# Performance work log

Measured on AMD Instinct MI355X. Metric: run time of the kernel, lower is better.

## Reference

```python
import jax, jax.numpy as jnp
import numpy as np

BN_EPS = 1e-5

def setup_inputs() -> dict:
    key = jax.random.key(0)
    k1, k2, k3 = jax.random.split(key, 3)
    N, F, H, E = 50000, 256, 256, 1600000
    x = jax.random.normal(k1, (N, F), dtype=jnp.float32)
    edge_index = jax.random.randint(k2, (2, E), 0, N, dtype=jnp.int64)
    # Linear(F, H) params, PyTorch default init scale
    lim = 1.0 / np.sqrt(F)
    W = jax.random.uniform(k3, (H, F), dtype=jnp.float32, minval=-lim, maxval=lim)
    b = jnp.zeros((H,), dtype=jnp.float32)
    bn_w = jnp.ones((H,), dtype=jnp.float32)
    bn_b = jnp.zeros((H,), dtype=jnp.float32)
    return {"x": x, "edge_index": edge_index, "W": W, "b": b, "bn_w": bn_w, "bn_b": bn_b}

def reference(x, edge_index, W, b, bn_w, bn_b):
    N = x.shape[0]
    src, dst = edge_index[0], edge_index[1]
    # GIN aggregation: sum of neighbor features (messages flow src -> dst)
    agg = jax.ops.segment_sum(x[src], dst, num_segments=N)
    h = x + agg  # (1 + eps) * x + agg, eps = 0
    # MLP: Linear then BatchNorm1d (training mode: batch stats, biased var)
    h = jnp.einsum('nf,hf->nh', h, W) + b
    mean = jnp.mean(h, axis=0)
    var = jnp.mean(jnp.square(h - mean), axis=0)
    out = (h - mean) * jax.lax.rsqrt(var + BN_EPS) * bn_w + bn_b
    return out
```

## Files before the change

kernel.cpp:

```cpp
#include <hip/hip_runtime.h>

#define NN 50000
#define FDIM 256
#define HDIM 256
#define BN_EPS 1e-5f
#define RB 32
#define KC 16
#define NP 264
#define SCAN_CHUNK 1024
#define NBLK_SCAN ((NN + SCAN_CHUNK - 1) / SCAN_CHUNK)

#define BKT 32
#define NBKT 1563
#define ECAP 1280
#define PFB 256
#define SBUF_CAP 6400
#define PSC_NPT 7
#define PAIR_SRC(p) (((p) >> 5) & 0xFFFFu)
#define PAIR_LDST(p) ((p) & 31u)

typedef __attribute__((ext_vector_type(8))) short short8v;
typedef __attribute__((ext_vector_type(8))) unsigned short ushort8v;
typedef __attribute__((ext_vector_type(4))) float f32x4;

__device__ __forceinline__ float b2f(unsigned short u) {
    return __uint_as_float(((unsigned)u) << 16);
}
__device__ __forceinline__ unsigned short f2b(float f) {
    unsigned u = __float_as_uint(f);
    return (unsigned short)((u + 0x7FFFu + ((u >> 16) & 1u)) >> 16);
}

__global__ void k_cvt2(const float4* __restrict__ x, const float4* __restrict__ W,
                       ushort4* __restrict__ xb, ushort4* __restrict__ Wb,
                       int nx4, int nw4) {
    int i = blockIdx.x * blockDim.x + threadIdx.x;
    if (i < nx4) {
        float4 v = x[i];
        xb[i] = make_ushort4(f2b(v.x), f2b(v.y), f2b(v.z), f2b(v.w));
    } else {
        int j = i - nx4;
        if (j < nw4) {
            float4 v = W[j];
            Wb[j] = make_ushort4(f2b(v.x), f2b(v.y), f2b(v.z), f2b(v.w));
        }
    }
}

__launch_bounds__(256)
__global__ void k_phist(const int* __restrict__ dst, int* __restrict__ bcnt, int E) {
    __shared__ int lhist[NBKT];
    int t = threadIdx.x;
    int chunk = (E + 255) / 256;
    int c0 = blockIdx.x * chunk;
    int c1 = min(E, c0 + chunk);
    for (int i = t; i < NBKT; i += 256) lhist[i] = 0;
    __syncthreads();
    for (int e = c0 + t; e < c1; e += 256) atomicAdd(&lhist[dst[e] >> 5], 1);
    __syncthreads();
    for (int i = t; i < NBKT; i += 256) {
        int h = lhist[i];
        if (h) atomicAdd(&bcnt[i], h);
    }
}

__global__ void k_pscan(const int* __restrict__ bcnt, int* __restrict__ bbase,
                        int* __restrict__ bcursor) {
    __shared__ int ts[256];
    int t = threadIdx.x;
    int i0 = t * PSC_NPT;
    int s = 0;
    for (int i = 0; i < PSC_NPT; i++) {
        int idx = i0 + i;
        if (idx < NBKT) s += bcnt[idx];
    }
    ts[t] = s;
    __syncthreads();
    for (int off = 1; off < 256; off <<= 1) {
        int val = (t >= off) ? ts[t - off] : 0;
        __syncthreads();
        ts[t] += val;
        __syncthreads();
    }
    int run = ts[t] - s;
    for (int i = 0; i < PSC_NPT; i++) {
        int idx = i0 + i;
        if (idx < NBKT) {
            bbase[idx] = run;
            bcursor[idx] = run;
            run += bcnt[idx];
        }
    }
}

__launch_bounds__(256)
__global__ void k_pfill_sort(const int* __restrict__ src, const int* __restrict__ dst,
                             int* __restrict__ bcursor, unsigned int* __restrict__ pairs,
                             int E) {
    __shared__ int lhist[NBKT];
    __shared__ int lofs[NBKT];
    __shared__ int ts[256];
    __shared__ unsigned int sbuf[SBUF_CAP];
    int t = threadIdx.x;
    int chunk = (E + PFB - 1) / PFB;
    int c0 = blockIdx.x * chunk;
    int c1 = min(E, c0 + chunk);
    int n = c1 - c0;

    for (int i = t; i < NBKT; i += 256) lhist[i] = 0;
    __syncthreads();
    for (int e = c0 + t; e < c1; e += 256) atomicAdd(&lhist[dst[e] >> 5], 1);
    __syncthreads();
    {
        int i0 = t * PSC_NPT;
        int s = 0;
        int loc[PSC_NPT];
        for (int i = 0; i < PSC_NPT; i++) {
            int idx = i0 + i;
            loc[i] = (idx < NBKT) ? lhist[idx] : 0;
            s += loc[i];
        }
        ts[t] = s;
        __syncthreads();
        for (int off = 1; off < 256; off <<= 1) {
            int val = (t >= off) ? ts[t - off] : 0;
            __syncthreads();
            ts[t] += val;
            __syncthreads();
        }
        int run = ts[t] - s;
        for (int i = 0; i < PSC_NPT; i++) {
            int idx = i0 + i;
            if (idx < NBKT) {
                lofs[idx] = run;
                run += loc[i];
            }
        }
    }
    __syncthreads();
    if (t < 256) {}
    for (int i = t; i < NBKT; i += 256) lhist[i] = lofs[i];
    __syncthreads();
    for (int e = c0 + t; e < c1; e += 256) {
        int d = dst[e];
        unsigned bkt = (unsigned)d >> 5;
        int rank = atomicAdd(&lhist[bkt], 1);
        sbuf[rank] = (bkt << 21) | ((unsigned)src[e] << 5) | ((unsigned)d & 31u);
    }
    __syncthreads();
    for (int i = t; i < NBKT; i += 256) {
        int cnt = lhist[i] - lofs[i];
        int gb = cnt ? atomicAdd(&bcursor[i], cnt) : 0;
        lhist[i] = gb - lofs[i];
    }
    __syncthreads();
    for (int j = t; j < n; j += 256) {
        unsigned int p = sbuf[j];
        pairs[j + lhist[p >> 21]] = p;
    }
}

__launch_bounds__(256)
__global__ void k_pfill(const int* __restrict__ src, const int* __restrict__ dst,
                        int* __restrict__ bcursor, unsigned int* __restrict__ pairs, int E) {
    __shared__ int lhist[NBKT];
    __shared__ int lbase[NBKT];
    int t = threadIdx.x;
    int chunk = (E + PFB - 1) / PFB;
    int c0 = blockIdx.x * chunk;
    int c1 = min(E, c0 + chunk);
    for (int i = t; i < NBKT; i += 256) lhist[i] = 0;
    __syncthreads();
    for (int e = c0 + t; e < c1; e += 256) atomicAdd(&lhist[dst[e] >> 5], 1);
    __syncthreads();
    for (int i = t; i < NBKT; i += 256) {
        int h = lhist[i];
        lbase[i] = h ? atomicAdd(&bcursor[i], h) : 0;
        lhist[i] = 0;
    }
    __syncthreads();
    for (int e = c0 + t; e < c1; e += 256) {
        int d = dst[e];
        unsigned bkt = (unsigned)d >> 5;
        int rank = atomicAdd(&lhist[bkt], 1);
        pairs[lbase[bkt] + rank] = (bkt << 21) | ((unsigned)src[e] << 5) | ((unsigned)d & 31u);
    }
}

__launch_bounds__(256, 6)
__global__ void k_agg_gemm(const ushort4* __restrict__ xb4, const unsigned int* __restrict__ pairs,
                           const int* __restrict__ bbase, const int* __restrict__ bcnt,
                           const unsigned short* __restrict__ Wb, const float* __restrict__ bias,
                           unsigned short* __restrict__ hb, float* __restrict__ stat) {
    __shared__ unsigned int lp[ECAP];
    __shared__ int lhist[BKT];
    __shared__ int lofs[BKT + 1];
    __shared__ unsigned short As[BKT * NP];
    __shared__ float ssum[HDIM];
    __shared__ float ssq[HDIM];
    const int t = threadIdx.x;
    const int lane = t & 63;
    const int wid = t >> 6;
    const int q = lane >> 4;
    const int l16 = lane & 15;
    const int v0 = blockIdx.x * BKT;
    const int ebeg = bbase[blockIdx.x];
    const int ecnt = bcnt[blockIdx.x];
    const int vrows = min(BKT, NN - v0);

    ssum[t] = 0.f;
    ssq[t] = 0.f;

    if (ecnt <= ECAP) {
        if (t < BKT) lhist[t] = 0;
        __syncthreads();
        for (int e = t; e < ecnt; e += 256)
            atomicAdd(&lhist[PAIR_LDST(pairs[ebeg + e])], 1);
        __syncthreads();
        if (t == 0) {
            int run = 0;
            for (int r = 0; r < BKT; r++) { lofs[r] = run; run += lhist[r]; }
            lofs[BKT] = run;
        }
        __syncthreads();
        if (t < BKT) lhist[t] = lofs[t];
        __syncthreads();
        for (int e = t; e < ecnt; e += 256) {
            unsigned int p = pairs[ebeg + e];
            int pos = atomicAdd(&lhist[PAIR_LDST(p)], 1);
            lp[pos] = p;
        }
        __syncthreads();
#pragma unroll
        for (int i = 0; i < 8; i++) {
            int r = wid * 8 + i;
            int v = v0 + r;
            if (v < NN) {
                ushort4 u0 = xb4[(size_t)v * 64 + lane];
                float a0 = b2f(u0.x), a1 = b2f(u0.y), a2 = b2f(u0.z), a3 = b2f(u0.w);
                int e0 = __builtin_amdgcn_readfirstlane(lofs[r]);
                int e1 = __builtin_amdgcn_readfirstlane(lofs[r + 1]);
                int e = e0;
                for (; e + 16 <= e1; e += 16) {
                    ushort4 u[16];
#pragma unroll
                    for (int j = 0; j < 16; j++)
                        u[j] = xb4[(size_t)PAIR_SRC(lp[e + j]) * 64 + lane];
#pragma unroll
                    for (int j = 0; j < 16; j++) {
                        a0 += b2f(u[j].x); a1 += b2f(u[j].y);
                        a2 += b2f(u[j].z); a3 += b2f(u[j].w);
                    }
                }
                for (; e + 4 <= e1; e += 4) {
                    ushort4 ua = xb4[(size_t)PAIR_SRC(lp[e]) * 64 + lane];
                    ushort4 ub = xb4[(size_t)PAIR_SRC(lp[e + 1]) * 64 + lane];
                    ushort4 uc = xb4[(size_t)PAIR_SRC(lp[e + 2]) * 64 + lane];
                    ushort4 ud = xb4[(size_t)PAIR_SRC(lp[e + 3]) * 64 + lane];
                    a0 += (b2f(ua.x) + b2f(ub.x)) + (b2f(uc.x) + b2f(ud.x));
                    a1 += (b2f(ua.y) + b2f(ub.y)) + (b2f(uc.y) + b2f(ud.y));
                    a2 += (b2f(ua.z) + b2f(ub.z)) + (b2f(uc.z) + b2f(ud.z));
                    a3 += (b2f(ua.w) + b2f(ub.w)) + (b2f(uc.w) + b2f(ud.w));
                }
                for (; e < e1; e++) {
                    ushort4 ua = xb4[(size_t)PAIR_SRC(lp[e]) * 64 + lane];
                    a0 += b2f(ua.x); a1 += b2f(ua.y); a2 += b2f(ua.z); a3 += b2f(ua.w);
                }
                *(ushort4*)(As + r * NP + lane * 4) =
                    make_ushort4(f2b(a0), f2b(a1), f2b(a2), f2b(a3));
            } else {
                *(ushort4*)(As + r * NP + lane * 4) = make_ushort4(0, 0, 0, 0);
            }
        }
    } else {
#pragma unroll
        for (int i = 0; i < 8; i++) {
            int r = wid * 8 + i;
            int v = v0 + r;
            float a0 = 0.f, a1 = 0.f, a2 = 0.f, a3 = 0.f;
            if (v < NN) {
                ushort4 u0 = xb4[(size_t)v * 64 + lane];
                a0 = b2f(u0.x); a1 = b2f(u0.y); a2 = b2f(u0.z); a3 = b2f(u0.w);
                for (int e = 0; e < ecnt; e++) {
                    unsigned int p = pairs[ebeg + e];
                    if ((int)PAIR_LDST(p) == r) {
                        ushort4 cu = xb4[(size_t)PAIR_SRC(p) * 64 + lane];
                        a0 += b2f(cu.x); a1 += b2f(cu.y); a2 += b2f(cu.z); a3 += b2f(cu.w);
                    }
                }
            }
            *(ushort4*)(As + r * NP + lane * 4) =
                make_ushort4(f2b(a0), f2b(a1), f2b(a2), f2b(a3));
        }
    }
    __syncthreads();

    f32x4 acc[2][4];
#pragma unroll
    for (int mt = 0; mt < 2; mt++)
#pragma unroll
        for (int nt = 0; nt < 4; nt++) acc[mt][nt] = (f32x4)0.f;

    const int w = wid;
#pragma unroll
    for (int ks = 0; ks < 8; ks++) {
        const int kk = ks * 32;
        short8v af[2], bf_[4];
#pragma unroll
        for (int mt = 0; mt < 2; mt++)
            af[mt] = *(const short8v*)(As + (mt * 16 + l16) * NP + kk + q * 8);
#pragma unroll
        for (int nt = 0; nt < 4; nt++)
            bf_[nt] = *(const short8v*)(Wb + (size_t)(w * 64 + nt * 16 + l16) * FDIM + kk + q * 8);
#pragma unroll
        for (int mt = 0; mt < 2; mt++)
#pragma unroll
            for (int nt = 0; nt < 4; nt++)
                acc[mt][nt] = __builtin_amdgcn_mfma_f32_16x16x32_bf16(af[mt], bf_[nt], acc[mt][nt], 0, 0, 0);
    }

#pragma unroll
    for (int nt = 0; nt < 4; nt++) {
        const int col = w * 64 + nt * 16 + l16;
        const float bcol = bias[col];
        float s = 0.f, qq = 0.f;
#pragma unroll
        for (int mt = 0; mt < 2; mt++) {
            const int rbase = mt * 16 + q * 4;
#pragma unroll
            for (int r = 0; r < 4; r++) {
                int row = rbase + r;
                if (row < vrows) {
                    float v = acc[mt][nt][r] + bcol;
                    hb[(size_t)(v0 + row) * FDIM + col] = f2b(v);
                    s += v;
                    qq += v * v;
                }
            }
        }
        atomicAdd(&ssum[col], s);
        atomicAdd(&ssq[col], qq);
    }
    __syncthreads();
    atomicAdd(&stat[t], ssum[t]);
    atomicAdd(&stat[256 + t], ssq[t]);
}

__global__ void k_final(const float* __restrict__ stat, const float* __restrict__ bn_w,
                        const float* __restrict__ bn_b, float* __restrict__ ss) {
    int j = threadIdx.x;
    const float inv_n = 1.0f / (float)NN;
    float mean = stat[j] * inv_n;
    float var = stat[256 + j] * inv_n - mean * mean;
    float sc = bn_w[j] * rsqrtf(var + BN_EPS);
    ss[j] = sc;
    ss[256 + j] = bn_b[j] - mean * sc;
}

__global__ void k_norm8(const ushort8v* __restrict__ hb8, const float* __restrict__ ss,
                        float4* __restrict__ out, int n8) {
    int i = blockIdx.x * blockDim.x + threadIdx.x;
    if (i >= n8) return;
    ushort8v u = hb8[i];
    int c8 = (i & 31) << 3;
    float4 sc0 = *(const float4*)(ss + c8);
    float4 sc1 = *(const float4*)(ss + c8 + 4);
    float4 sh0 = *(const float4*)(ss + 256 + c8);
    float4 sh1 = *(const float4*)(ss + 256 + c8 + 4);
    float4 v0, v1;
    v0.x = fmaf(b2f(u[0]), sc0.x, sh0.x);
    v0.y = fmaf(b2f(u[1]), sc0.y, sh0.y);
    v0.z = fmaf(b2f(u[2]), sc0.z, sh0.z);
    v0.w = fmaf(b2f(u[3]), sc0.w, sh0.w);
    v1.x = fmaf(b2f(u[4]), sc1.x, sh1.x);
    v1.y = fmaf(b2f(u[5]), sc1.y, sh1.y);
    v1.z = fmaf(b2f(u[6]), sc1.z, sh1.z);
    v1.w = fmaf(b2f(u[7]), sc1.w, sh1.w);
    out[i * 2 + 0] = v0;
    out[i * 2 + 1] = v1;
}

__global__ void k_hist(const int* __restrict__ dst, int* __restrict__ cnt, int E) {
    int e = blockIdx.x * blockDim.x + threadIdx.x;
    if (e < E) atomicAdd(&cnt[dst[e]], 1);
}
__global__ void k_scan1(const int* __restrict__ cnt, int* __restrict__ offs,
                        int* __restrict__ bsum) {
    __shared__ int ts[256];
    int t = threadIdx.x;
    int base = blockIdx.x * SCAN_CHUNK + t * 4;
    int v0 = (base + 0 < NN) ? cnt[base + 0] : 0;
    int v1 = (base + 1 < NN) ? cnt[base + 1] : 0;
    int v2 = (base + 2 < NN) ? cnt[base + 2] : 0;
    int v3 = (base + 3 < NN) ? cnt[base + 3] : 0;
    int tsum = v0 + v1 + v2 + v3;
    ts[t] = tsum;
    __syncthreads();
    for (int off = 1; off < 256; off <<= 1) {
        int val = (t >= off) ? ts[t - off] : 0;
        __syncthreads();
        ts[t] += val;
        __syncthreads();
    }
    int excl = ts[t] - tsum;
    if (t == 255) bsum[blockIdx.x] = ts[255];
    if (base + 0 < NN) offs[base + 0] = excl;
    if (base + 1 < NN) offs[base + 1] = excl + v0;
    if (base + 2 < NN) offs[base + 2] = excl + v0 + v1;
    if (base + 3 < NN) offs[base + 3] = excl + v0 + v1 + v2;
}
__global__ void k_scan2(int* __restrict__ bsum, int nb) {
    if (threadIdx.x == 0 && blockIdx.x == 0) {
        int run = 0;
        for (int i = 0; i < nb; i++) { int v = bsum[i]; bsum[i] = run; run += v; }
    }
}
__global__ void k_scan3(int* __restrict__ offs, const int* __restrict__ bsum,
                        int* __restrict__ cursor) {
    int i = blockIdx.x * blockDim.x + threadIdx.x;
    if (i >= NN) return;
    int o = offs[i] + bsum[i >> 10];
    offs[i] = o;
    cursor[i] = o;
}
__global__ void k_bucket(const int* __restrict__ src, const int* __restrict__ dst,
                         int* __restrict__ cursor, int* __restrict__ csr, int E) {
    int e = blockIdx.x * blockDim.x + threadIdx.x;
    if (e >= E) return;
    int pos = atomicAdd(&cursor[dst[e]], 1);
    csr[pos] = src[e];
}
__global__ void k_copy(const float4* __restrict__ x, float4* __restrict__ out, int n4) {
    int i = blockIdx.x * blockDim.x + threadIdx.x;
    if (i < n4) out[i] = x[i];
}
__global__ void k_scatter(const float* __restrict__ x, const int* __restrict__ src,
                          const int* __restrict__ dst, float* __restrict__ out, int E) {
    int t = blockIdx.x * blockDim.x + threadIdx.x;
    int e = t >> 6;
    if (e >= E) return;
    int c = (t & 63) << 2;
    long s = src[e], d = dst[e];
    const float4 v = *(const float4*)(x + s * FDIM + c);
    float* o = out + d * FDIM + c;
    atomicAdd(o + 0, v.x);
    atomicAdd(o + 1, v.y);
    atomicAdd(o + 2, v.z);
    atomicAdd(o + 3, v.w);
}
__launch_bounds__(256)
__global__ void k_gather(const float4* __restrict__ x, const int* __restrict__ offs,
                         const int* __restrict__ cnt, const int* __restrict__ csr,
                         float4* __restrict__ out) {
    int v = blockIdx.x * 4 + (threadIdx.x >> 6);
    if (v >= NN) return;
    int lane = threadIdx.x & 63;
    int beg = __builtin_amdgcn_readfirstlane(offs[v]);
    int d   = __builtin_amdgcn_readfirstlane(cnt[v]);
    float4 acc = x[(size_t)v * 64 + lane];
    int i = 0;
    for (; i + 4 <= d; i += 4) {
        int s0 = csr[beg + i], s1 = csr[beg + i + 1];
        int s2 = csr[beg + i + 2], s3 = csr[beg + i + 3];
        float4 a = x[(size_t)s0 * 64 + lane];
        float4 b = x[(size_t)s1 * 64 + lane];
        float4 c = x[(size_t)s2 * 64 + lane];
        float4 e = x[(size_t)s3 * 64 + lane];
        acc.x += (a.x + b.x) + (c.x + e.x);
        acc.y += (a.y + b.y) + (c.y + e.y);
        acc.z += (a.z + b.z) + (c.z + e.z);
        acc.w += (a.w + b.w) + (c.w + e.w);
    }
    for (; i < d; i++) {
        int s = csr[beg + i];
        float4 a = x[(size_t)s * 64 + lane];
        acc.x += a.x; acc.y += a.y; acc.z += a.z; acc.w += a.w;
    }
    out[(size_t)v * 64 + lane] = acc;
}
__launch_bounds__(256)
__global__ void k_gemm_stats(float* __restrict__ h,
                             const float* __restrict__ W,
                             const float* __restrict__ bias,
                             float* __restrict__ stat) {
    __shared__ float hs[RB * FDIM];
    __shared__ float wt[KC * HDIM];
    const int j = threadIdx.x;
    const int c = j & 63;
    const int g = j >> 6;
    const long row0 = (long)blockIdx.x * RB;
    const int vrows = min(RB, NN - (int)row0);
    const int vf4 = vrows * (FDIM / 4);

    float4* hsv = (float4*)hs;
    const float4* hv = (const float4*)(h + row0 * FDIM);
#pragma unroll
    for (int i = 0; i < (RB * FDIM / 4) / 256; i++) {
        int f4 = j + i * 256;
        hsv[f4] = (f4 < vf4) ? hv[f4] : make_float4(0.f, 0.f, 0.f, 0.f);
    }
    __syncthreads();

    float acc[8][4];
#pragma unroll
    for (int r = 0; r < 8; r++)
#pragma unroll
        for (int qi = 0; qi < 4; qi++) acc[r][qi] = 0.f;

    for (int kb = 0; kb < FDIM; kb += KC) {
        __syncthreads();
#pragma unroll
        for (int i = 0; i < KC / 4; i++) {
            float4 w4 = *(const float4*)(W + (size_t)j * FDIM + kb + i * 4);
            wt[(i * 4 + 0) * HDIM + j] = w4.x;
            wt[(i * 4 + 1) * HDIM + j] = w4.y;
            wt[(i * 4 + 2) * HDIM + j] = w4.z;
            wt[(i * 4 + 3) * HDIM + j] = w4.w;
        }
        __syncthreads();
#pragma unroll
        for (int k = 0; k < KC; k++) {
            float4 wv = *(const float4*)(wt + k * HDIM + c * 4);
#pragma unroll
            for (int r = 0; r < 8; r++) {
                float hval = hs[(g * 8 + r) * FDIM + kb + k];
                acc[r][0] = fmaf(hval, wv.x, acc[r][0]);
                acc[r][1] = fmaf(hval, wv.y, acc[r][1]);
                acc[r][2] = fmaf(hval, wv.z, acc[r][2]);
                acc[r][3] = fmaf(hval, wv.w, acc[r][3]);
            }
        }
    }
    __syncthreads();
    wt[j] = 0.f;
    wt[256 + j] = 0.f;
    __syncthreads();

    float4 bv = *(const float4*)(bias + c * 4);
    float s0 = 0, s1 = 0, s2 = 0, s3 = 0, q0 = 0, q1 = 0, q2 = 0, q3 = 0;
#pragma unroll
    for (int r = 0; r < 8; r++) {
        int row = g * 8 + r;
        if (row < vrows) {
            float4 v;
            v.x = acc[r][0] + bv.x;
            v.y = acc[r][1] + bv.y;
            v.z = acc[r][2] + bv.z;
            v.w = acc[r][3] + bv.w;
            *(float4*)(h + (row0 + row) * FDIM + c * 4) = v;
            s0 += v.x; s1 += v.y; s2 += v.z; s3 += v.w;
            q0 += v.x * v.x; q1 += v.y * v.y; q2 += v.z * v.z; q3 += v.w * v.w;
        }
    }
    atomicAdd(&wt[c * 4 + 0], s0);
    atomicAdd(&wt[c * 4 + 1], s1);
    atomicAdd(&wt[c * 4 + 2], s2);
    atomicAdd(&wt[c * 4 + 3], s3);
    atomicAdd(&wt[256 + c * 4 + 0], q0);
    atomicAdd(&wt[256 + c * 4 + 1], q1);
    atomicAdd(&wt[256 + c * 4 + 2], q2);
    atomicAdd(&wt[256 + c * 4 + 3], q3);
    __syncthreads();
    atomicAdd(&stat[j], wt[j]);
    atomicAdd(&stat[256 + j], wt[256 + j]);
}
__global__ void k_norm(float* __restrict__ out, const float* __restrict__ ss, int n4) {
    int i = blockIdx.x * blockDim.x + threadIdx.x;
    if (i >= n4) return;
    float4 v = ((float4*)out)[i];
    int c4 = (i & 63) << 2;
    float4 sc = *(const float4*)(ss + c4);
    float4 sh = *(const float4*)(ss + 256 + c4);
    v.x = fmaf(v.x, sc.x, sh.x);
    v.y = fmaf(v.y, sc.y, sh.y);
    v.z = fmaf(v.z, sc.z, sh.z);
    v.w = fmaf(v.w, sc.w, sh.w);
    ((float4*)out)[i] = v;
}

extern "C" void kernel_launch(void* const* d_in, const int* in_sizes, int n_in,
                              void* d_out, int out_size, void* d_ws, size_t ws_size,
                              hipStream_t stream) {
    const float* x   = (const float*)d_in[0];
    const int*   ei  = (const int*)d_in[1];
    const float* W   = (const float*)d_in[2];
    const float* b   = (const float*)d_in[3];
    const float* bnw = (const float*)d_in[4];
    const float* bnb = (const float*)d_in[5];
    float* out = (float*)d_out;
    char* ws = (char*)d_ws;
    const int E = in_sizes[1] / 2;
    const int n4 = NN * FDIM / 4;
    const int n8 = NN * FDIM / 8;
    const int* src = ei;
    const int* dst = ei + E;

    size_t off = 0;
    float* stat = (float*)(ws + off);          off += 4096;
    int* bcnt   = (int*)(ws + off);            off += 8192;
    int* bbase  = (int*)(ws + off);            off += 8192;
    int* bcur   = (int*)(ws + off);            off += 8192;
    unsigned int* pairs = (unsigned int*)(ws + off); off += (size_t)E * 4;
    off = (off + 255) & ~(size_t)255;
    unsigned short* Wb = (unsigned short*)(ws + off); off += 131072;
    unsigned short* xb = (unsigned short*)(ws + off); off += (size_t)NN * FDIM * 2;
    unsigned short* hb = (unsigned short*)(ws + off); off += (size_t)NN * FDIM * 2;
    const size_t need_fast = off;

    size_t foff = 0;
    float* fstat  = (float*)(ws + foff); foff += 4096;
    int*   cnt    = (int*)(ws + foff);   foff += 204800;
    int*   offs   = (int*)(ws + foff);   foff += 204800;
    int*   cursor = (int*)(ws + foff);   foff += 204800;
    int*   bsum   = (int*)(ws + foff);   foff += 4096;
    int*   csr    = (int*)(ws + foff);   foff += (size_t)E * 4;
    const size_t need_mid = foff;

    const bool src_fits = (NN <= 65536);

    if (ws_size >= need_fast && src_fits) {
        hipMemsetAsync(stat, 0, 2 * 256 * sizeof(float), stream);
        hipMemsetAsync(bcnt, 0, NBKT * sizeof(int), stream);
        const int nw4 = HDIM * FDIM / 4;
        k_cvt2<<<(n4 + nw4 + 255) / 256, 256, 0, stream>>>((const float4*)x, (const float4*)W,
                                                           (ushort4*)xb, (ushort4*)Wb, n4, nw4);
        k_phist<<<256, 256, 0, stream>>>(dst, bcnt, E);
        k_pscan<<<1, 256, 0, stream>>>(bcnt, bbase, bcur);
        const int chunk = (E + PFB - 1) / PFB;
        if (chunk <= SBUF_CAP)
            k_pfill_sort<<<PFB, 256, 0, stream>>>(src, dst, bcur, pairs, E);
        else
            k_pfill<<<PFB, 256, 0, stream>>>(src, dst, bcur, pairs, E);
        k_agg_gemm<<<NBKT, 256, 0, stream>>>((const ushort4*)xb, pairs, bbase, bcnt,
                                             Wb, b, hb, stat);
        k_final<<<1, 256, 0, stream>>>(stat, bnw, bnb, stat + 512);
        k_norm8<<<(n8 + 255) / 256, 256, 0, stream>>>((const ushort8v*)hb, stat + 512,
                                                      (float4*)out, n8);
    } else if (ws_size >= need_mid) {
        hipMemsetAsync(fstat, 0, 2 * 256 * sizeof(float), stream);
        hipMemsetAsync(cnt, 0, NN * sizeof(int), stream);
        k_hist<<<(E + 255) / 256, 256, 0, stream>>>(dst, cnt, E);
        k_scan1<<<NBLK_SCAN, 256, 0, stream>>>(cnt, offs, bsum);
        k_scan2<<<1, 64, 0, stream>>>(bsum, NBLK_SCAN);
        k_scan3<<<(NN + 255) / 256, 256, 0, stream>>>(offs, bsum, cursor);
        k_bucket<<<(E + 255) / 256, 256, 0, stream>>>(src, dst, cursor, csr, E);
        k_gather<<<(NN + 3) / 4, 256, 0, stream>>>((const float4*)x, offs, cnt, csr,
                                                   (float4*)out);
        k_gemm_stats<<<(NN + RB - 1) / RB, 256, 0, stream>>>(out, W, b, fstat);
        k_final<<<1, 256, 0, stream>>>(fstat, bnw, bnb, fstat + 512);
        k_norm<<<(n4 + 255) / 256, 256, 0, stream>>>(out, fstat + 512, n4);
    } else {
        hipMemsetAsync(fstat, 0, 2 * 256 * sizeof(float), stream);
        k_copy<<<(n4 + 255) / 256, 256, 0, stream>>>((const float4*)x, (float4*)out, n4);
        long threads = (long)E * 64;
        k_scatter<<<(int)((threads + 255) / 256), 256, 0, stream>>>(x, src, dst, out, E);
        k_gemm_stats<<<(NN + RB - 1) / RB, 256, 0, stream>>>(out, W, b, fstat);
        k_final<<<1, 256, 0, stream>>>(fstat, bnw, bnb, fstat + 512);
        k_norm<<<(n4 + 255) / 256, 256, 0, stream>>>(out, fstat + 512, n4);
    }
}
```

Before: 326.6 us.

## Split fused aggregate-GEMM into CSR column-sliced gather plus separate MFMA GEMM

Adds a new default path that builds a per-node CSR through hist/scan/bucket, then gathers neighbor rows in 32-column slices so each block touches only a slice of xb, which is meant to improve cache reuse. A separate bf16 MFMA GEMM kernel computes the batch-norm statistics. The memsets are folded into the conversion kernel and scan2 now stages through shared memory. The cost is an extra round trip of the aggregated bf16 hb buffer through memory and atomic-based bucketing in place of the bucketed pair sort.

```diff
diff --git a/kernel.cpp b/kernel.cpp
--- a/kernel.cpp
+++ b/kernel.cpp
@@ -19,9 +19,13 @@
 #define PAIR_SRC(p) (((p) >> 5) & 0xFFFFu)
 #define PAIR_LDST(p) ((p) & 31u)
 
+#define NSLC 8
+#define AGG_BLOCKS 1536
+
 typedef __attribute__((ext_vector_type(8))) short short8v;
 typedef __attribute__((ext_vector_type(8))) unsigned short ushort8v;
 typedef __attribute__((ext_vector_type(4))) float f32x4;
+typedef __attribute__((ext_vector_type(4))) unsigned short us4;
 
 __device__ __forceinline__ float b2f(unsigned short u) {
     return __uint_as_float(((unsigned)u) << 16);
@@ -45,6 +49,239 @@
             Wb[j] = make_ushort4(f2b(v.x), f2b(v.y), f2b(v.z), f2b(v.w));
         }
     }
+}
+
+__global__ void k_cvt2z(const float4* __restrict__ x, const float4* __restrict__ W,
+                        ushort4* __restrict__ xb, ushort4* __restrict__ Wb,
+                        int nx4, int nw4, float* __restrict__ stat, int* __restrict__ cnt) {
+    int i = blockIdx.x * blockDim.x + threadIdx.x;
+    if (i < NN) cnt[i] = 0;
+    if (i < 512) stat[i] = 0.f;
+    if (i < nx4) {
+        float4 v = x[i];
+        xb[i] = make_ushort4(f2b(v.x), f2b(v.y), f2b(v.z), f2b(v.w));
+    } else {
+        int j = i - nx4;
+        if (j < nw4) {
+            float4 v = W[j];
+            Wb[j] = make_ushort4(f2b(v.x), f2b(v.y), f2b(v.z), f2b(v.w));
+        }
+    }
+}
+
+__global__ void k_hist(const int* __restrict__ dst, int* __restrict__ cnt, int E) {
+    int e = blockIdx.x * blockDim.x + threadIdx.x;
+    if (e < E) atomicAdd(&cnt[dst[e]], 1);
+}
+__global__ void k_scan1(const int* __restrict__ cnt, int* __restrict__ offs,
+                        int* __restrict__ bsum) {
+    __shared__ int ts[256];
+    int t = threadIdx.x;
+    int base = blockIdx.x * SCAN_CHUNK + t * 4;
+    int v0 = (base + 0 < NN) ? cnt[base + 0] : 0;
+    int v1 = (base + 1 < NN) ? cnt[base + 1] : 0;
+    int v2 = (base + 2 < NN) ? cnt[base + 2] : 0;
+    int v3 = (base + 3 < NN) ? cnt[base + 3] : 0;
+    int tsum = v0 + v1 + v2 + v3;
+    ts[t] = tsum;
+    __syncthreads();
+    for (int off = 1; off < 256; off <<= 1) {
+        int val = (t >= off) ? ts[t - off] : 0;
+        __syncthreads();
+        ts[t] += val;
+        __syncthreads();
+    }
+    int excl = ts[t] - tsum;
+    if (t == 255) bsum[blockIdx.x] = ts[255];
+    if (base + 0 < NN) offs[base + 0] = excl;
+    if (base + 1 < NN) offs[base + 1] = excl + v0;
+    if (base + 2 < NN) offs[base + 2] = excl + v0 + v1;
+    if (base + 3 < NN) offs[base + 3] = excl + v0 + v1 + v2;
+}
+__global__ void k_scan2(int* __restrict__ bsum, int nb) {
+    __shared__ int s[64];
+    int t = threadIdx.x;
+    s[t] = (t < nb) ? bsum[t] : 0;
+    __syncthreads();
+    if (t == 0) {
+        int run = 0;
+        for (int i = 0; i < nb; i++) { int v = s[i]; s[i] = run; run += v; }
+    }
+    __syncthreads();
+    if (t < nb) bsum[t] = s[t];
+}
+__global__ void k_scan3(int* __restrict__ offs, const int* __restrict__ bsum,
+                        int* __restrict__ cursor, int E) {
+    int i = blockIdx.x * blockDim.x + threadIdx.x;
+    if (i == 0) offs[NN] = E;
+    if (i >= NN) return;
+    int o = offs[i] + bsum[i >> 10];
+    offs[i] = o;
+    cursor[i] = o;
+}
+__global__ void k_bucket(const int* __restrict__ src, const int* __restrict__ dst,
+                         int* __restrict__ cursor, int* __restrict__ csr, int E) {
+    int e = blockIdx.x * blockDim.x + threadIdx.x;
+    if (e >= E) return;
+    int pos = atomicAdd(&cursor[dst[e]], 1);
+    csr[pos] = src[e];
+}
+
+__launch_bounds__(256, 6)
+__global__ void k_agg_slice(const unsigned short* __restrict__ xb,
+                            const int* __restrict__ srcs,
+                            const int* __restrict__ offs,
+                            unsigned short* __restrict__ hb) {
+    const int t = threadIdx.x;
+    const int lane = t & 63;
+    const int wid = t >> 6;
+    const int sg = lane >> 3;
+    const int qd = lane & 7;
+    const int slice = blockIdx.x & 7;
+    const int cb = slice * 32 + qd * 4;
+    const int nper = gridDim.x >> 3;
+    for (int tile = blockIdx.x >> 3; tile < NBKT; tile += nper) {
+        const int v = tile * BKT + wid * 8 + sg;
+        if (v >= NN) continue;
+        ushort4 u0 = *(const ushort4*)(xb + ((size_t)v << 8) + cb);
+        float a0 = b2f(u0.x), a1 = b2f(u0.y), a2 = b2f(u0.z), a3 = b2f(u0.w);
+        int e = offs[v];
+        const int e1 = offs[v + 1];
+        for (; e + 8 <= e1; e += 8) {
+            int s[8];
+#pragma unroll
+            for (int j = 0; j < 8; j++) s[j] = __builtin_nontemporal_load(srcs + e + j);
+            ushort4 u[8];
+#pragma unroll
+            for (int j = 0; j < 8; j++)
+                u[j] = *(const ushort4*)(xb + ((size_t)s[j] << 8) + cb);
+#pragma unroll
+            for (int j = 0; j < 8; j++) {
+                a0 += b2f(u[j].x); a1 += b2f(u[j].y);
+                a2 += b2f(u[j].z); a3 += b2f(u[j].w);
+            }
+        }
+        for (; e < e1; e++) {
+            int s0 = __builtin_nontemporal_load(srcs + e);
+            ushort4 ua = *(const ushort4*)(xb + ((size_t)s0 << 8) + cb);
+            a0 += b2f(ua.x); a1 += b2f(ua.y); a2 += b2f(ua.z); a3 += b2f(ua.w);
+        }
+        us4 o;
+        o.x = f2b(a0); o.y = f2b(a1); o.z = f2b(a2); o.w = f2b(a3);
+        __builtin_nontemporal_store(o, (us4*)(hb + ((size_t)v << 8) + cb));
+    }
+}
+
+__launch_bounds__(256, 6)
+__global__ void k_gemm_bn(unsigned short* __restrict__ hb,
+                          const unsigned short* __restrict__ Wb,
+                          const float* __restrict__ bias,
+                          float* __restrict__ stat) {
+    __shared__ unsigned short As[BKT * NP];
+    __shared__ float ssum[HDIM];
+    __shared__ float ssq[HDIM];
+    const int t = threadIdx.x;
+    const int lane = t & 63;
+    const int wid = t >> 6;
+    const int q = lane >> 4;
+    const int l16 = lane & 15;
+    const int v0 = blockIdx.x * BKT;
+    const int vrows = min(BKT, NN - v0);
+    ssum[t] = 0.f;
+    ssq[t] = 0.f;
+#pragma unroll
+    for (int i = 0; i < 8; i++) {
+        int r = wid * 8 + i;
+        int v = v0 + r;
+        ushort4 u = (v < NN) ? ((const ushort4*)hb)[(size_t)v * 64 + lane]
+                             : make_ushort4(0, 0, 0, 0);
+        *(ushort4*)(As + r * NP + lane * 4) = u;
+    }
+    __syncthreads();
+
+    f32x4 acc[2][4];
+#pragma unroll
+    for (int mt = 0; mt < 2; mt++)
+#pragma unroll
+        for (int nt = 0; nt < 4; nt++) acc[mt][nt] = (f32x4)0.f;
+
+    const int w = wid;
+#pragma unroll
+    for (int ks = 0; ks < 8; ks++) {
+        const int kk = ks * 32;
+        short8v af[2], bf_[4];
+#pragma unroll
+        for (int mt = 0; mt < 2; mt++)
+            af[mt] = *(const short8v*)(As + (mt * 16 + l16) * NP + kk + q * 8);
+#pragma unroll
+        for (int nt = 0; nt < 4; nt++)
+            bf_[nt] = *(const short8v*)(Wb + (size_t)(w * 64 + nt * 16 + l16) * FDIM + kk + q * 8);
+#pragma unroll
+        for (int mt = 0; mt < 2; mt++)
+#pragma unroll
+            for (int nt = 0; nt < 4; nt++)
+                acc[mt][nt] = __builtin_amdgcn_mfma_f32_16x16x32_bf16(af[mt], bf_[nt], acc[mt][nt], 0, 0, 0);
+    }
+
+#pragma unroll
+    for (int nt = 0; nt < 4; nt++) {
+        const int col = w * 64 + nt * 16 + l16;
+        const float bcol = bias[col];
+        float s = 0.f, qq = 0.f;
+#pragma unroll
+        for (int mt = 0; mt < 2; mt++) {
+            const int rbase = mt * 16 + q * 4;
+#pragma unroll
+            for (int r = 0; r < 4; r++) {
+                int row = rbase + r;
+                if (row < vrows) {
+                    float v = acc[mt][nt][r] + bcol;
+                    hb[(size_t)(v0 + row) * FDIM + col] = f2b(v);
+                    s += v;
+                    qq += v * v;
+                }
+            }
+        }
+        atomicAdd(&ssum[col], s);
+        atomicAdd(&ssq[col], qq);
+    }
+    __syncthreads();
+    atomicAdd(&stat[t], ssum[t]);
+    atomicAdd(&stat[256 + t], ssq[t]);
+}
+
+__global__ void k_final(const float* __restrict__ stat, const float* __restrict__ bn_w,
+                        const float* __restrict__ bn_b, float* __restrict__ ss) {
+    int j = threadIdx.x;
+    const float inv_n = 1.0f / (float)NN;
+    float mean = stat[j] * inv_n;
+    float var = stat[256 + j] * inv_n - mean * mean;
+    float sc = bn_w[j] * rsqrtf(var + BN_EPS);
+    ss[j] = sc;
+    ss[256 + j] = bn_b[j] - mean * sc;
+}
+
+__global__ void k_norm8(const ushort8v* __restrict__ hb8, const float* __restrict__ ss,
+                        float4* __restrict__ out, int n8) {
+    int i = blockIdx.x * blockDim.x + threadIdx.x;
+    if (i >= n8) return;
+    ushort8v u = hb8[i];
+    int c8 = (i & 31) << 3;
+    float4 sc0 = *(const float4*)(ss + c8);
+    float4 sc1 = *(const float4*)(ss + c8 + 4);
+    float4 sh0 = *(const float4*)(ss + 256 + c8);
+    float4 sh1 = *(const float4*)(ss + 256 + c8 + 4);
+    float4 v0, v1;
+    v0.x = fmaf(b2f(u[0]), sc0.x, sh0.x);
+    v0.y = fmaf(b2f(u[1]), sc0.y, sh0.y);
+    v0.z = fmaf(b2f(u[2]), sc0.z, sh0.z);
+    v0.w = fmaf(b2f(u[3]), sc0.w, sh0.w);
+    v1.x = fmaf(b2f(u[4]), sc1.x, sh1.x);
+    v1.y = fmaf(b2f(u[5]), sc1.y, sh1.y);
+    v1.z = fmaf(b2f(u[6]), sc1.z, sh1.z);
+    v1.w = fmaf(b2f(u[7]), sc1.w, sh1.w);
+    out[i * 2 + 0] = v0;
+    out[i * 2 + 1] = v1;
 }
 
 __launch_bounds__(256)
@@ -138,7 +375,6 @@
         }
     }
     __syncthreads();
-    if (t < 256) {}
     for (int i = t; i < NBKT; i += 256) lhist[i] = lofs[i];
     __syncthreads();
     for (int e = c0 + t; e < c1; e += 256) {
@@ -346,90 +582,6 @@
     atomicAdd(&stat[256 + t], ssq[t]);
 }
 
-__global__ void k_final(const float* __restrict__ stat, const float* __restrict__ bn_w,
-                        const float* __restrict__ bn_b, float* __restrict__ ss) {
-    int j = threadIdx.x;
-    const float inv_n = 1.0f / (float)NN;
-    float mean = stat[j] * inv_n;
-    float var = stat[256 + j] * inv_n - mean * mean;
-    float sc = bn_w[j] * rsqrtf(var + BN_EPS);
-    ss[j] = sc;
-    ss[256 + j] = bn_b[j] - mean * sc;
-}
-
-__global__ void k_norm8(const ushort8v* __restrict__ hb8, const float* __restrict__ ss,
-                        float4* __restrict__ out, int n8) {
-    int i = blockIdx.x * blockDim.x + threadIdx.x;
-    if (i >= n8) return;
-    ushort8v u = hb8[i];
-    int c8 = (i & 31) << 3;
-    float4 sc0 = *(const float4*)(ss + c8);
-    float4 sc1 = *(const float4*)(ss + c8 + 4);
-    float4 sh0 = *(const float4*)(ss + 256 + c8);
-    float4 sh1 = *(const float4*)(ss + 256 + c8 + 4);
-    float4 v0, v1;
-    v0.x = fmaf(b2f(u[0]), sc0.x, sh0.x);
-    v0.y = fmaf(b2f(u[1]), sc0.y, sh0.y);
-    v0.z = fmaf(b2f(u[2]), sc0.z, sh0.z);
-    v0.w = fmaf(b2f(u[3]), sc0.w, sh0.w);
-    v1.x = fmaf(b2f(u[4]), sc1.x, sh1.x);
-    v1.y = fmaf(b2f(u[5]), sc1.y, sh1.y);
-    v1.z = fmaf(b2f(u[6]), sc1.z, sh1.z);
-    v1.w = fmaf(b2f(u[7]), sc1.w, sh1.w);
-    out[i * 2 + 0] = v0;
-    out[i * 2 + 1] = v1;
-}
-
-__global__ void k_hist(const int* __restrict__ dst, int* __restrict__ cnt, int E) {
-    int e = blockIdx.x * blockDim.x + threadIdx.x;
-    if (e < E) atomicAdd(&cnt[dst[e]], 1);
-}
-__global__ void k_scan1(const int* __restrict__ cnt, int* __restrict__ offs,
-                        int* __restrict__ bsum) {
-    __shared__ int ts[256];
-    int t = threadIdx.x;
-    int base = blockIdx.x * SCAN_CHUNK + t * 4;
-    int v0 = (base + 0 < NN) ? cnt[base + 0] : 0;
-    int v1 = (base + 1 < NN) ? cnt[base + 1] : 0;
-    int v2 = (base + 2 < NN) ? cnt[base + 2] : 0;
-    int v3 = (base + 3 < NN) ? cnt[base + 3] : 0;
-    int tsum = v0 + v1 + v2 + v3;
-    ts[t] = tsum;
-    __syncthreads();
-    for (int off = 1; off < 256; off <<= 1) {
-        int val = (t >= off) ? ts[t - off] : 0;
-        __syncthreads();
-        ts[t] += val;
-        __syncthreads();
-    }
-    int excl = ts[t] - tsum;
-    if (t == 255) bsum[blockIdx.x] = ts[255];
-    if (base + 0 < NN) offs[base + 0] = excl;
-    if (base + 1 < NN) offs[base + 1] = excl + v0;
-    if (base + 2 < NN) offs[base + 2] = excl + v0 + v1;
-    if (base + 3 < NN) offs[base + 3] = excl + v0 + v1 + v2;
-}
-__global__ void k_scan2(int* __restrict__ bsum, int nb) {
-    if (threadIdx.x == 0 && blockIdx.x == 0) {
-        int run = 0;
-        for (int i = 0; i < nb; i++) { int v = bsum[i]; bsum[i] = run; run += v; }
-    }
-}
-__global__ void k_scan3(int* __restrict__ offs, const int* __restrict__ bsum,
-                        int* __restrict__ cursor) {
-    int i = blockIdx.x * blockDim.x + threadIdx.x;
-    if (i >= NN) return;
-    int o = offs[i] + bsum[i >> 10];
-    offs[i] = o;
-    cursor[i] = o;
-}
-__global__ void k_bucket(const int* __restrict__ src, const int* __restrict__ dst,
-                         int* __restrict__ cursor, int* __restrict__ csr, int E) {
-    int e = blockIdx.x * blockDim.x + threadIdx.x;
-    if (e >= E) return;
-    int pos = atomicAdd(&cursor[dst[e]], 1);
-    csr[pos] = src[e];
-}
 __global__ void k_copy(const float4* __restrict__ x, float4* __restrict__ out, int n4) {
     int i = blockIdx.x * blockDim.x + threadIdx.x;
     if (i < n4) out[i] = x[i];
@@ -595,6 +747,20 @@
     const int* src = ei;
     const int* dst = ei + E;
 
+    size_t f2 = 0;
+    float* fstat  = (float*)(ws + f2); f2 += 4096;
+    int*   cnt    = (int*)(ws + f2);   f2 += 204800;
+    int*   offs   = (int*)(ws + f2);   f2 += 204800;
+    int*   cursor = (int*)(ws + f2);   f2 += 204800;
+    int*   bsum   = (int*)(ws + f2);   f2 += 4096;
+    int*   csr    = (int*)(ws + f2);   f2 += (size_t)E * 4;
+    const size_t need_mid = f2;
+    f2 = (f2 + 255) & ~(size_t)255;
+    unsigned short* Wb2 = (unsigned short*)(ws + f2); f2 += 131072;
+    unsigned short* xb2 = (unsigned short*)(ws + f2); f2 += (size_t)NN * FDIM * 2;
+    unsigned short* hb2 = (unsigned short*)(ws + f2); f2 += (size_t)NN * FDIM * 2;
+    const size_t need_fast2 = f2;
+
     size_t off = 0;
     float* stat = (float*)(ws + off);          off += 4096;
     int* bcnt   = (int*)(ws + off);            off += 8192;
@@ -607,21 +773,26 @@
     unsigned short* hb = (unsigned short*)(ws + off); off += (size_t)NN * FDIM * 2;
     const size_t need_fast = off;
 
-    size_t foff = 0;
-    float* fstat  = (float*)(ws + foff); foff += 4096;
-    int*   cnt    = (int*)(ws + foff);   foff += 204800;
-    int*   offs   = (int*)(ws + foff);   foff += 204800;
-    int*   cursor = (int*)(ws + foff);   foff += 204800;
-    int*   bsum   = (int*)(ws + foff);   foff += 4096;
-    int*   csr    = (int*)(ws + foff);   foff += (size_t)E * 4;
-    const size_t need_mid = foff;
-
     const bool src_fits = (NN <= 65536);
-
-    if (ws_size >= need_fast && src_fits) {
+    const int nw4 = HDIM * FDIM / 4;
+
+    if (ws_size >= need_fast2) {
+        k_cvt2z<<<(n4 + nw4 + 255) / 256, 256, 0, stream>>>((const float4*)x, (const float4*)W,
+                                                            (ushort4*)xb2, (ushort4*)Wb2,
+                                                            n4, nw4, fstat, cnt);
+        k_hist<<<(E + 255) / 256, 256, 0, stream>>>(dst, cnt, E);
+        k_scan1<<<NBLK_SCAN, 256, 0, stream>>>(cnt, offs, bsum);
+        k_scan2<<<1, 64, 0, stream>>>(bsum, NBLK_SCAN);
+        k_scan3<<<(NN + 255) / 256, 256, 0, stream>>>(offs, bsum, cursor, E);
+        k_bucket<<<(E + 255) / 256, 256, 0, stream>>>(src, dst, cursor, csr, E);
+        k_agg_slice<<<AGG_BLOCKS, 256, 0, stream>>>(xb2, csr, offs, hb2);
+        k_gemm_bn<<<NBKT, 256, 0, stream>>>(hb2, Wb2, b, fstat);
+        k_final<<<1, 256, 0, stream>>>(fstat, bnw, bnb, fstat + 512);
+        k_norm8<<<(n8 + 255) / 256, 256, 0, stream>>>((const ushort8v*)hb2, fstat + 512,
+                                                      (float4*)out, n8);
+    } else if (ws_size >= need_fast && src_fits) {
         hipMemsetAsync(stat, 0, 2 * 256 * sizeof(float), stream);
         hipMemsetAsync(bcnt, 0, NBKT * sizeof(int), stream);
-        const int nw4 = HDIM * FDIM / 4;
         k_cvt2<<<(n4 + nw4 + 255) / 256, 256, 0, stream>>>((const float4*)x, (const float4*)W,
                                                            (ushort4*)xb, (ushort4*)Wb, n4, nw4);
         k_phist<<<256, 256, 0, stream>>>(dst, bcnt, E);
@@ -642,7 +813,7 @@
         k_hist<<<(E + 255) / 256, 256, 0, stream>>>(dst, cnt, E);
         k_scan1<<<NBLK_SCAN, 256, 0, stream>>>(cnt, offs, bsum);
         k_scan2<<<1, 64, 0, stream>>>(bsum, NBLK_SCAN);
-        k_scan3<<<(NN + 255) / 256, 256, 0, stream>>>(offs, bsum, cursor);
+        k_scan3<<<(NN + 255) / 256, 256, 0, stream>>>(offs, bsum, cursor, E);
         k_bucket<<<(E + 255) / 256, 256, 0, stream>>>(src, dst, cursor, csr, E);
         k_gather<<<(NN + 3) / 4, 256, 0, stream>>>((const float4*)x, offs, cnt, csr,
                                                    (float4*)out);
```

Result: slower. 598.9 us (+83.4%).

## Fuse conversion with bucket histogram and use plain fill with more blocks

Applied to the files above, without the earlier changes.

Merges the bf16 conversion kernel and the bucket histogram kernel into one launch, with the first 256 blocks doing the histogram and the rest doing the conversion. The two memsets become a single memset over the workspace head. The shared-memory locally-sorted pair fill is dropped in favour of the simpler direct-scatter fill launched with 1024 blocks instead of 256. The serial scan2 now stages its data in shared memory. This trades launch count and shared-memory pressure against less coalesced scatter writes in the fill, and the single memset assumes stat and bcnt both lie in the first 12288 bytes of the workspace.

```diff
diff --git a/kernel.cpp b/kernel.cpp
--- a/kernel.cpp
+++ b/kernel.cpp
@@ -13,8 +13,7 @@
 #define BKT 32
 #define NBKT 1563
 #define ECAP 1280
-#define PFB 256
-#define SBUF_CAP 6400
+#define PFB2 1024
 #define PSC_NPT 7
 #define PAIR_SRC(p) (((p) >> 5) & 0xFFFFu)
 #define PAIR_LDST(p) ((p) & 31u)
@@ -31,36 +30,38 @@
     return (unsigned short)((u + 0x7FFFu + ((u >> 16) & 1u)) >> 16);
 }
 
-__global__ void k_cvt2(const float4* __restrict__ x, const float4* __restrict__ W,
-                       ushort4* __restrict__ xb, ushort4* __restrict__ Wb,
-                       int nx4, int nw4) {
-    int i = blockIdx.x * blockDim.x + threadIdx.x;
-    if (i < nx4) {
-        float4 v = x[i];
-        xb[i] = make_ushort4(f2b(v.x), f2b(v.y), f2b(v.z), f2b(v.w));
+__launch_bounds__(256)
+__global__ void k_cvthist(const float4* __restrict__ x, const float4* __restrict__ W,
+                          ushort4* __restrict__ xb, ushort4* __restrict__ Wb,
+                          int nx4, int nw4,
+                          const int* __restrict__ dst, int* __restrict__ bcnt, int E) {
+    const int bid = blockIdx.x;
+    const int t = threadIdx.x;
+    if (bid < 256) {
+        __shared__ int lhist[NBKT];
+        int chunk = (E + 255) / 256;
+        int c0 = bid * chunk;
+        int c1 = min(E, c0 + chunk);
+        for (int i = t; i < NBKT; i += 256) lhist[i] = 0;
+        __syncthreads();
+        for (int e = c0 + t; e < c1; e += 256) atomicAdd(&lhist[dst[e] >> 5], 1);
+        __syncthreads();
+        for (int i = t; i < NBKT; i += 256) {
+            int h = lhist[i];
+            if (h) atomicAdd(&bcnt[i], h);
+        }
     } else {
-        int j = i - nx4;
-        if (j < nw4) {
-            float4 v = W[j];
-            Wb[j] = make_ushort4(f2b(v.x), f2b(v.y), f2b(v.z), f2b(v.w));
-        }
-    }
-}
-
-__launch_bounds__(256)
-__global__ void k_phist(const int* __restrict__ dst, int* __restrict__ bcnt, int E) {
-    __shared__ int lhist[NBKT];
-    int t = threadIdx.x;
-    int chunk = (E + 255) / 256;
-    int c0 = blockIdx.x * chunk;
-    int c1 = min(E, c0 + chunk);
-    for (int i = t; i < NBKT; i += 256) lhist[i] = 0;
-    __syncthreads();
-    for (int e = c0 + t; e < c1; e += 256) atomicAdd(&lhist[dst[e] >> 5], 1);
-    __syncthreads();
-    for (int i = t; i < NBKT; i += 256) {
-        int h = lhist[i];
-        if (h) atomicAdd(&bcnt[i], h);
+        int i = (bid - 256) * 256 + t;
+        if (i < nx4) {
+            float4 v = x[i];
+            xb[i] = make_ushort4(f2b(v.x), f2b(v.y), f2b(v.z), f2b(v.w));
+        } else {
+            int j = i - nx4;
+            if (j < nw4) {
+                float4 v = W[j];
+                Wb[j] = make_ushort4(f2b(v.x), f2b(v.y), f2b(v.z), f2b(v.w));
+            }
+        }
     }
 }
 
@@ -94,79 +95,12 @@
 }
 
 __launch_bounds__(256)
-__global__ void k_pfill_sort(const int* __restrict__ src, const int* __restrict__ dst,
-                             int* __restrict__ bcursor, unsigned int* __restrict__ pairs,
-                             int E) {
-    __shared__ int lhist[NBKT];
-    __shared__ int lofs[NBKT];
-    __shared__ int ts[256];
-    __shared__ unsigned int sbuf[SBUF_CAP];
-    int t = threadIdx.x;
-    int chunk = (E + PFB - 1) / PFB;
-    int c0 = blockIdx.x * chunk;
-    int c1 = min(E, c0 + chunk);
-    int n = c1 - c0;
-
-    for (int i = t; i < NBKT; i += 256) lhist[i] = 0;
-    __syncthreads();
-    for (int e = c0 + t; e < c1; e += 256) atomicAdd(&lhist[dst[e] >> 5], 1);
-    __syncthreads();
-    {
-        int i0 = t * PSC_NPT;
-        int s = 0;
-        int loc[PSC_NPT];
-        for (int i = 0; i < PSC_NPT; i++) {
-            int idx = i0 + i;
-            loc[i] = (idx < NBKT) ? lhist[idx] : 0;
-            s += loc[i];
-        }
-        ts[t] = s;
-        __syncthreads();
-        for (int off = 1; off < 256; off <<= 1) {
-            int val = (t >= off) ? ts[t - off] : 0;
-            __syncthreads();
-            ts[t] += val;
-            __syncthreads();
-        }
-        int run = ts[t] - s;
-        for (int i = 0; i < PSC_NPT; i++) {
-            int idx = i0 + i;
-            if (idx < NBKT) {
-                lofs[idx] = run;
-                run += loc[i];
-            }
-        }
-    }
-    __syncthreads();
-    if (t < 256) {}
-    for (int i = t; i < NBKT; i += 256) lhist[i] = lofs[i];
-    __syncthreads();
-    for (int e = c0 + t; e < c1; e += 256) {
-        int d = dst[e];
-        unsigned bkt = (unsigned)d >> 5;
-        int rank = atomicAdd(&lhist[bkt], 1);
-        sbuf[rank] = (bkt << 21) | ((unsigned)src[e] << 5) | ((unsigned)d & 31u);
-    }
-    __syncthreads();
-    for (int i = t; i < NBKT; i += 256) {
-        int cnt = lhist[i] - lofs[i];
-        int gb = cnt ? atomicAdd(&bcursor[i], cnt) : 0;
-        lhist[i] = gb - lofs[i];
-    }
-    __syncthreads();
-    for (int j = t; j < n; j += 256) {
-        unsigned int p = sbuf[j];
-        pairs[j + lhist[p >> 21]] = p;
-    }
-}
-
-__launch_bounds__(256)
 __global__ void k_pfill(const int* __restrict__ src, const int* __restrict__ dst,
                         int* __restrict__ bcursor, unsigned int* __restrict__ pairs, int E) {
     __shared__ int lhist[NBKT];
     __shared__ int lbase[NBKT];
     int t = threadIdx.x;
-    int chunk = (E + PFB - 1) / PFB;
+    int chunk = (E + PFB2 - 1) / PFB2;
     int c0 = blockIdx.x * chunk;
     int c1 = min(E, c0 + chunk);
     for (int i = t; i < NBKT; i += 256) lhist[i] = 0;
@@ -410,10 +344,16 @@
     if (base + 3 < NN) offs[base + 3] = excl + v0 + v1 + v2;
 }
 __global__ void k_scan2(int* __restrict__ bsum, int nb) {
-    if (threadIdx.x == 0 && blockIdx.x == 0) {
+    __shared__ int s[64];
+    int t = threadIdx.x;
+    s[t] = (t < nb) ? bsum[t] : 0;
+    __syncthreads();
+    if (t == 0) {
         int run = 0;
-        for (int i = 0; i < nb; i++) { int v = bsum[i]; bsum[i] = run; run += v; }
-    }
+        for (int i = 0; i < nb; i++) { int v = s[i]; s[i] = run; run += v; }
+    }
+    __syncthreads();
+    if (t < nb) bsum[t] = s[t];
 }
 __global__ void k_scan3(int* __restrict__ offs, const int* __restrict__ bsum,
                         int* __restrict__ cursor) {
@@ -617,20 +557,16 @@
     const size_t need_mid = foff;
 
     const bool src_fits = (NN <= 65536);
+    const int nw4 = HDIM * FDIM / 4;
 
     if (ws_size >= need_fast && src_fits) {
-        hipMemsetAsync(stat, 0, 2 * 256 * sizeof(float), stream);
-        hipMemsetAsync(bcnt, 0, NBKT * sizeof(int), stream);
-        const int nw4 = HDIM * FDIM / 4;
-        k_cvt2<<<(n4 + nw4 + 255) / 256, 256, 0, stream>>>((const float4*)x, (const float4*)W,
-                                                           (ushort4*)xb, (ushort4*)Wb, n4, nw4);
-        k_phist<<<256, 256, 0, stream>>>(dst, bcnt, E);
+        hipMemsetAsync(ws, 0, 12288, stream);
+        const int ncvt = (n4 + nw4 + 255) / 256;
+        k_cvthist<<<ncvt + 256, 256, 0, stream>>>((const float4*)x, (const float4*)W,
+                                                  (ushort4*)xb, (ushort4*)Wb, n4, nw4,
+                                                  dst, bcnt, E);
         k_pscan<<<1, 256, 0, stream>>>(bcnt, bbase, bcur);
-        const int chunk = (E + PFB - 1) / PFB;
-        if (chunk <= SBUF_CAP)
-            k_pfill_sort<<<PFB, 256, 0, stream>>>(src, dst, bcur, pairs, E);
-        else
-            k_pfill<<<PFB, 256, 0, stream>>>(src, dst, bcur, pairs, E);
+        k_pfill<<<PFB2, 256, 0, stream>>>(src, dst, bcur, pairs, E);
         k_agg_gemm<<<NBKT, 256, 0, stream>>>((const ushort4*)xb, pairs, bbase, bcnt,
                                              Wb, b, hb, stat);
         k_final<<<1, 256, 0, stream>>>(stat, bnw, bnb, stat + 512);
```

After: 340.9 us. +4.4%, slower.
